# Kernel tuning notes

Hardware: AMD Instinct MI355X
Metric: run time of the kernel (lower is better)

## Reference

```python
import jax, jax.numpy as jnp
import numpy as np

N = 4  # hypercomplex dimension

def setup_inputs() -> dict:
    key = jax.random.key(0)
    k1, k2, k3 = jax.random.split(key, 3)
    x = jax.random.normal(k1, (32, 196, 768), dtype=jnp.float32)
    # [n, out_pad/n, in_pad/n] = [4, 3072//4, 768//4]
    weight_components = jax.random.normal(k2, (N, 768, 192), dtype=jnp.float32) * 0.02
    bias = jax.random.normal(k3, (3072,), dtype=jnp.float32) * 0.02
    return {"x": x, "weight_components": weight_components, "bias": bias}

def reference(x, weight_components, bias):
    n, out_blk, in_blk = weight_components.shape
    batch_shape = x.shape[:-1]
    xb = x.reshape(-1, n, in_blk)  # [B, n, in_blk]
    # original: out[:, (i+j)%n] += x[:, j] @ W[i].T
    # equivalently out[:, k] = sum_j x[:, j] @ W[(k-j)%n].T
    k_idx = jnp.arange(n)[:, None]
    j_idx = jnp.arange(n)[None, :]
    Wperm = weight_components[(k_idx - j_idx) % n]  # [n(k), n(j), out_blk, in_blk]
    out = jnp.einsum('bjc,kjoc->bko', xb, Wperm)    # [B, n, out_blk]
    out = out.reshape(-1, n * out_blk) + bias
    return out.reshape(*batch_shape, n * out_blk)
```

## Files before the change

kernel.cpp:

```cpp
#include <hip/hip_runtime.h>
#include <stdint.h>

#define M_ROWS 6272
#define K_DIM  768
#define N_DIM  3072
#define BM 128
#define BN 256
#define BK 32
#define NITER (K_DIM / BK)

#define X_CHUNKS (M_ROWS * K_DIM / 8)
#define W_CHUNKS (N_DIM * K_DIM / 8)
#define X_BLOCKS (X_CHUNKS / 256)
#define W_BLOCKS (W_CHUNKS / 256)

#define GRID_X (N_DIM / BN)
#define GRID_Y (M_ROWS / BM)
#define NWG    (GRID_X * GRID_Y)

typedef unsigned short u16;
typedef __attribute__((ext_vector_type(8))) __bf16 bf16x8;
typedef __attribute__((ext_vector_type(4))) float f32x4;

__device__ __forceinline__ u16 f32_to_bf16(float f) {
    unsigned u = __float_as_uint(f);
    unsigned r = 0x7FFFu + ((u >> 16) & 1u);
    return (u16)((u + r) >> 16);
}

__device__ __forceinline__ unsigned pack2(float a, float b) {
    return (unsigned)f32_to_bf16(a) | ((unsigned)f32_to_bf16(b) << 16);
}

__device__ __forceinline__ void lds_barrier() {
    asm volatile("s_waitcnt lgkmcnt(0)\n\ts_barrier" ::: "memory");
}

__global__ void prep_kernel(const float* __restrict__ x, const float* __restrict__ w,
                            u16* __restrict__ xb, u16* __restrict__ wb) {
    int b = blockIdx.x;
    if (b < X_BLOCKS) {
        int idx = b * 256 + threadIdx.x;
        const float4* xp = (const float4*)x + (size_t)idx * 2;
        float4 a = xp[0], c = xp[1];
        uint4 v;
        v.x = pack2(a.x, a.y);
        v.y = pack2(a.z, a.w);
        v.z = pack2(c.x, c.y);
        v.w = pack2(c.z, c.w);
        ((uint4*)xb)[idx] = v;
    } else {
        int idx = (b - X_BLOCKS) * 256 + threadIdx.x;
        int n    = idx / 96;
        int kc   = idx - n * 96;
        int kblk = n / 768;
        int o    = n - kblk * 768;
        int j    = kc / 24;
        int c8   = kc - j * 24;
        int i    = (kblk - j) & 3;
        const float* src = w + (((size_t)i * 768 + o) * 192 + c8 * 8);
        float4 a = ((const float4*)src)[0];
        float4 c = ((const float4*)src)[1];
        uint4 v;
        v.x = pack2(a.x, a.y);
        v.y = pack2(a.z, a.w);
        v.z = pack2(c.x, c.y);
        v.w = pack2(c.z, c.w);
        ((uint4*)wb)[idx] = v;
    }
}

__global__ __launch_bounds__(512, 4) void gemm_bt(
    const u16* __restrict__ A,
    const u16* __restrict__ B,
    const float* __restrict__ bias,
    float* __restrict__ C)
{
    __shared__ __align__(16) u16 As[2][BM * BK];
    __shared__ __align__(16) u16 Bs[2][BN * BK];

    const int orig = blockIdx.x;
    const int xcd  = orig & 7;
    const int pos  = orig >> 3;
    const int q    = NWG >> 3;
    const int r    = NWG & 7;
    const int lin  = (xcd < r ? xcd * (q + 1) : r * (q + 1) + (xcd - r) * q) + pos;
    const int rowBlk = lin / GRID_X;
    const int colBlk = lin - rowBlk * GRID_X;

    const int rowBase = rowBlk * BM;
    const int colBase = colBlk * BN;

    const int tid    = threadIdx.x;
    const int wave   = tid >> 6;
    const int lane   = tid & 63;
    const int lane16 = lane & 15;
    const int quad   = lane >> 4;
    const int wr     = wave >> 2;
    const int wc     = wave & 3;

    const int cA  = tid;
    const int rA  = cA >> 2,  sA  = (cA & 3) ^ ((rA >> 1) & 3);
    const int cB0 = tid;
    const int cB1 = tid + 512;
    const int rB0 = cB0 >> 2, sB0 = (cB0 & 3) ^ ((rB0 >> 1) & 3);
    const int rB1 = cB1 >> 2, sB1 = (cB1 & 3) ^ ((rB1 >> 1) & 3);

    const uint4* Ag  = (const uint4*)(A + (size_t)(rowBase + rA) * K_DIM + sA * 8);
    const uint4* Bg0 = (const uint4*)(B + (size_t)(colBase + rB0) * K_DIM + sB0 * 8);
    const uint4* Bg1 = (const uint4*)(B + (size_t)(colBase + rB1) * K_DIM + sB1 * 8);
    uint4* Al  = (uint4*)&As[0][cA * 8];
    uint4* Bl0 = (uint4*)&Bs[0][cB0 * 8];
    uint4* Bl1 = (uint4*)&Bs[0][cB1 * 8];
    const int aBufStride = (BM * BK) / 8;
    const int bBufStride = (BN * BK) / 8;

    const int swz  = (lane16 >> 1) & 3;
    const int slot = (quad ^ swz) * 8;
    int aoff[4], boff[4];
#pragma unroll
    for (int i = 0; i < 4; ++i)
        aoff[i] = (wr * 64 + i * 16 + lane16) * BK + slot;
#pragma unroll
    for (int j = 0; j < 4; ++j)
        boff[j] = (wc * 64 + j * 16 + lane16) * BK + slot;

    f32x4 acc[4][4] = {};

    const int kStep = BK / 8;

    uint4 ga = Ag[0], gb0 = Bg0[0], gb1 = Bg1[0];
    Al[0] = ga; Bl0[0] = gb0; Bl1[0] = gb1;
    ga = Ag[kStep]; gb0 = Bg0[kStep]; gb1 = Bg1[kStep];
    lds_barrier();

#pragma unroll 2
    for (int it = 0; it < NITER - 2; ++it) {
        const int cur = it & 1, nxt = cur ^ 1;

        bf16x8 af[4], bfv[4];
#pragma unroll
        for (int i = 0; i < 4; ++i)
            af[i] = *(const bf16x8*)&As[cur][aoff[i]];
#pragma unroll
        for (int j = 0; j < 4; ++j)
            bfv[j] = *(const bf16x8*)&Bs[cur][boff[j]];
#pragma unroll
        for (int i = 0; i < 4; ++i)
#pragma unroll
            for (int j = 0; j < 4; ++j)
                acc[i][j] = __builtin_amdgcn_mfma_f32_16x16x32_bf16(
                    af[i], bfv[j], acc[i][j], 0, 0, 0);

        Al[nxt * aBufStride]  = ga;
        Bl0[nxt * bBufStride] = gb0;
        Bl1[nxt * bBufStride] = gb1;
        const int g = (it + 2) * kStep;
        ga = Ag[g]; gb0 = Bg0[g]; gb1 = Bg1[g];
        lds_barrier();
    }

    {
        const int cur = (NITER - 2) & 1, nxt = cur ^ 1;
        bf16x8 af[4], bfv[4];
#pragma unroll
        for (int i = 0; i < 4; ++i)
            af[i] = *(const bf16x8*)&As[cur][aoff[i]];
#pragma unroll
        for (int j = 0; j < 4; ++j)
            bfv[j] = *(const bf16x8*)&Bs[cur][boff[j]];
#pragma unroll
        for (int i = 0; i < 4; ++i)
#pragma unroll
            for (int j = 0; j < 4; ++j)
                acc[i][j] = __builtin_amdgcn_mfma_f32_16x16x32_bf16(
                    af[i], bfv[j], acc[i][j], 0, 0, 0);
        Al[nxt * aBufStride]  = ga;
        Bl0[nxt * bBufStride] = gb0;
        Bl1[nxt * bBufStride] = gb1;
        lds_barrier();
    }

    {
        const int cur = (NITER - 1) & 1;
        bf16x8 af[4], bfv[4];
#pragma unroll
        for (int i = 0; i < 4; ++i)
            af[i] = *(const bf16x8*)&As[cur][aoff[i]];
#pragma unroll
        for (int j = 0; j < 4; ++j)
            bfv[j] = *(const bf16x8*)&Bs[cur][boff[j]];
#pragma unroll
        for (int i = 0; i < 4; ++i)
#pragma unroll
            for (int j = 0; j < 4; ++j)
                acc[i][j] = __builtin_amdgcn_mfma_f32_16x16x32_bf16(
                    af[i], bfv[j], acc[i][j], 0, 0, 0);
    }

    float bv[4];
#pragma unroll
    for (int j = 0; j < 4; ++j)
        bv[j] = bias[colBase + wc * 64 + j * 16 + lane16];
#pragma unroll
    for (int i = 0; i < 4; ++i) {
        int row0 = rowBase + wr * 64 + i * 16 + quad * 4;
#pragma unroll
        for (int r2 = 0; r2 < 4; ++r2) {
            float* cp = C + (size_t)(row0 + r2) * N_DIM + colBase + wc * 64 + lane16;
#pragma unroll
            for (int j = 0; j < 4; ++j)
                cp[j * 16] = acc[i][j][r2] + bv[j];
        }
    }
}

extern "C" void kernel_launch(void* const* d_in, const int* in_sizes, int n_in,
                              void* d_out, int out_size, void* d_ws, size_t ws_size,
                              hipStream_t stream) {
    const float* x    = (const float*)d_in[0];
    const float* w    = (const float*)d_in[1];
    const float* bias = (const float*)d_in[2];
    float* out = (float*)d_out;

    u16* xb = (u16*)d_ws;
    u16* wb = (u16*)((char*)d_ws + (size_t)M_ROWS * K_DIM * 2);

    hipLaunchKernelGGL(prep_kernel, dim3(X_BLOCKS + W_BLOCKS), dim3(256),
                       0, stream, x, w, xb, wb);
    hipLaunchKernelGGL(gemm_bt, dim3(NWG), dim3(512),
                       0, stream, xb, wb, bias, out);
}
```

Measured before the change: 133.1 us.

## Use direct global-to-LDS loads with triple-buffered pipeline in GEMM

Replaces the register-staged global→LDS copies with global_load_lds (16-byte direct-to-LDS) transfers and moves from double to triple buffering. The loop is restructured so loads for stage k+2 are issued before waiting on stage k+1 via vmcnt. It also raises wave priority around the MFMA block with s_setprio. The goal is to remove VGPR staging and ds_write instructions and hide more memory latency. In exchange it uses more LDS (72KB vs 48KB per block), which may reduce occupancy from the requested 4 blocks per CU, and it relies on the direct-load lane layout matching the swizzled LDS layout.

Measured after the change: 136.2 us. 1.02x slower.

```diff
diff --git a/kernel.cpp b/kernel.cpp
--- a/kernel.cpp
+++ b/kernel.cpp
@@ -35,6 +35,10 @@
 __device__ __forceinline__ void lds_barrier() {
     asm volatile("s_waitcnt lgkmcnt(0)\n\ts_barrier" ::: "memory");
 }
+
+#define GLOAD16(gp, lp) __builtin_amdgcn_global_load_lds( \
+    (const __attribute__((address_space(1))) void*)(gp),  \
+    (__attribute__((address_space(3))) void*)(lp), 16, 0, 0)
 
 __global__ void prep_kernel(const float* __restrict__ x, const float* __restrict__ w,
                             u16* __restrict__ xb, u16* __restrict__ wb) {
@@ -76,8 +80,8 @@
     const float* __restrict__ bias,
     float* __restrict__ C)
 {
-    __shared__ __align__(16) u16 As[2][BM * BK];
-    __shared__ __align__(16) u16 Bs[2][BN * BK];
+    __shared__ __align__(16) u16 As[3][BM * BK];
+    __shared__ __align__(16) u16 Bs[3][BN * BK];
 
     const int orig = blockIdx.x;
     const int xcd  = orig & 7;
@@ -109,11 +113,15 @@
     const uint4* Ag  = (const uint4*)(A + (size_t)(rowBase + rA) * K_DIM + sA * 8);
     const uint4* Bg0 = (const uint4*)(B + (size_t)(colBase + rB0) * K_DIM + sB0 * 8);
     const uint4* Bg1 = (const uint4*)(B + (size_t)(colBase + rB1) * K_DIM + sB1 * 8);
-    uint4* Al  = (uint4*)&As[0][cA * 8];
-    uint4* Bl0 = (uint4*)&Bs[0][cB0 * 8];
-    uint4* Bl1 = (uint4*)&Bs[0][cB1 * 8];
-    const int aBufStride = (BM * BK) / 8;
-    const int bBufStride = (BN * BK) / 8;
+
+    char* AsB = (char*)As + wave * 1024;
+    char* BsB = (char*)Bs + wave * 1024;
+
+#define ISSUE(g, b) do {                                     \
+        GLOAD16(Ag  + (g) * 4, AsB + (b) * 8192);            \
+        GLOAD16(Bg0 + (g) * 4, BsB + (b) * 16384);           \
+        GLOAD16(Bg1 + (g) * 4, BsB + (b) * 16384 + 8192);    \
+    } while (0)
 
     const int swz  = (lane16 >> 1) & 3;
     const int slot = (quad ^ swz) * 8;
@@ -127,76 +135,56 @@
 
     f32x4 acc[4][4] = {};
 
-    const int kStep = BK / 8;
-
-    uint4 ga = Ag[0], gb0 = Bg0[0], gb1 = Bg1[0];
-    Al[0] = ga; Bl0[0] = gb0; Bl1[0] = gb1;
-    ga = Ag[kStep]; gb0 = Bg0[kStep]; gb1 = Bg1[kStep];
-    lds_barrier();
-
-#pragma unroll 2
-    for (int it = 0; it < NITER - 2; ++it) {
-        const int cur = it & 1, nxt = cur ^ 1;
-
-        bf16x8 af[4], bfv[4];
-#pragma unroll
-        for (int i = 0; i < 4; ++i)
-            af[i] = *(const bf16x8*)&As[cur][aoff[i]];
-#pragma unroll
-        for (int j = 0; j < 4; ++j)
-            bfv[j] = *(const bf16x8*)&Bs[cur][boff[j]];
-#pragma unroll
-        for (int i = 0; i < 4; ++i)
-#pragma unroll
-            for (int j = 0; j < 4; ++j)
-                acc[i][j] = __builtin_amdgcn_mfma_f32_16x16x32_bf16(
-                    af[i], bfv[j], acc[i][j], 0, 0, 0);
-
-        Al[nxt * aBufStride]  = ga;
-        Bl0[nxt * bBufStride] = gb0;
-        Bl1[nxt * bBufStride] = gb1;
-        const int g = (it + 2) * kStep;
-        ga = Ag[g]; gb0 = Bg0[g]; gb1 = Bg1[g];
-        lds_barrier();
-    }
-
-    {
-        const int cur = (NITER - 2) & 1, nxt = cur ^ 1;
-        bf16x8 af[4], bfv[4];
-#pragma unroll
-        for (int i = 0; i < 4; ++i)
-            af[i] = *(const bf16x8*)&As[cur][aoff[i]];
-#pragma unroll
-        for (int j = 0; j < 4; ++j)
-            bfv[j] = *(const bf16x8*)&Bs[cur][boff[j]];
-#pragma unroll
-        for (int i = 0; i < 4; ++i)
-#pragma unroll
-            for (int j = 0; j < 4; ++j)
-                acc[i][j] = __builtin_amdgcn_mfma_f32_16x16x32_bf16(
-                    af[i], bfv[j], acc[i][j], 0, 0, 0);
-        Al[nxt * aBufStride]  = ga;
-        Bl0[nxt * bBufStride] = gb0;
-        Bl1[nxt * bBufStride] = gb1;
-        lds_barrier();
-    }
-
-    {
-        const int cur = (NITER - 1) & 1;
-        bf16x8 af[4], bfv[4];
-#pragma unroll
-        for (int i = 0; i < 4; ++i)
-            af[i] = *(const bf16x8*)&As[cur][aoff[i]];
-#pragma unroll
-        for (int j = 0; j < 4; ++j)
-            bfv[j] = *(const bf16x8*)&Bs[cur][boff[j]];
-#pragma unroll
-        for (int i = 0; i < 4; ++i)
-#pragma unroll
-            for (int j = 0; j < 4; ++j)
-                acc[i][j] = __builtin_amdgcn_mfma_f32_16x16x32_bf16(
-                    af[i], bfv[j], acc[i][j], 0, 0, 0);
-    }
+#define DS_READS(cb)                                                        \
+    _Pragma("unroll") for (int i = 0; i < 4; ++i)                           \
+        af[i] = *(const bf16x8*)&As[cb][aoff[i]];                           \
+    _Pragma("unroll") for (int j = 0; j < 4; ++j)                           \
+        bfv[j] = *(const bf16x8*)&Bs[cb][boff[j]];
+
+#define MFMA16()                                                            \
+    __builtin_amdgcn_s_setprio(1);                                          \
+    _Pragma("unroll") for (int i = 0; i < 4; ++i)                           \
+    _Pragma("unroll") for (int j = 0; j < 4; ++j)                           \
+        acc[i][j] = __builtin_amdgcn_mfma_f32_16x16x32_bf16(                \
+            af[i], bfv[j], acc[i][j], 0, 0, 0);                             \
+    __builtin_amdgcn_s_setprio(0);
+
+#define ITER_ISSUE(cb, fb, g) {                                             \
+        bf16x8 af[4], bfv[4];                                               \
+        DS_READS(cb)                                                        \
+        ISSUE(g, fb);                                                       \
+        asm volatile("s_waitcnt vmcnt(3)" ::: "memory");                    \
+        lds_barrier();                                                      \
+        MFMA16()                                                            \
+    }
+
+#define ITER_DRAIN(cb) {                                                    \
+        bf16x8 af[4], bfv[4];                                               \
+        DS_READS(cb)                                                        \
+        asm volatile("s_waitcnt vmcnt(0)" ::: "memory");                    \
+        lds_barrier();                                                      \
+        MFMA16()                                                            \
+    }
+
+#define ITER_FINAL(cb) {                                                    \
+        bf16x8 af[4], bfv[4];                                               \
+        DS_READS(cb)                                                        \
+        MFMA16()                                                            \
+    }
+
+    ISSUE(0, 0);
+    ISSUE(1, 1);
+    asm volatile("s_waitcnt vmcnt(3)\n\ts_barrier" ::: "memory");
+
+    for (int t = 0; t < 7; ++t) {
+        const int g = t * 3;
+        ITER_ISSUE(0, 2, g + 2);
+        ITER_ISSUE(1, 0, g + 3);
+        ITER_ISSUE(2, 1, g + 4);
+    }
+    ITER_ISSUE(0, 2, 23);
+    ITER_DRAIN(1);
+    ITER_FINAL(2);
 
     float bv[4];
 #pragma unroll
@@ -213,6 +201,12 @@
                 cp[j * 16] = acc[i][j][r2] + bv[j];
         }
     }
+#undef ISSUE
+#undef DS_READS
+#undef MFMA16
+#undef ITER_ISSUE
+#undef ITER_DRAIN
+#undef ITER_FINAL
 }
 
 extern "C" void kernel_launch(void* const* d_in, const int* in_sizes, int n_in,
```
